# Optimization experiments

Hardware: AMD Instinct MI355X
Metric: run time of the kernel (lower is better)

Reference implementation:

```python
import jax, jax.numpy as jnp
import numpy as np

N = 200000
D = 128
PARAM_SCALE = 1.0 / D  # keep exp() exponent bounded (original torch.rand init overflows at scale)


def setup_inputs() -> dict:
    key = jax.random.key(0)
    kx, k1, k2, k3, k4 = jax.random.split(key, 5)
    X = jax.random.normal(kx, (N, D), dtype=jnp.float32)
    W_sum = jax.random.uniform(k1, (D, D), dtype=jnp.float32) * PARAM_SCALE
    W_alpha = jax.random.uniform(k2, (D, D), dtype=jnp.float32) * PARAM_SCALE
    a_alpha = jax.random.uniform(k3, (D, 1), dtype=jnp.float32) * PARAM_SCALE
    b_alpha = jax.random.uniform(k4, (D, 1), dtype=jnp.float32) * PARAM_SCALE
    return {"X": X, "W_sum": W_sum, "W_alpha": W_alpha,
            "a_alpha": a_alpha, "b_alpha": b_alpha}


def reference(X, W_sum, W_alpha, a_alpha, b_alpha):
    # a_w = a_alpha^T @ W_alpha, b_w = b_alpha^T @ W_alpha  -> (D,) each
    a_w = a_alpha[:, 0] @ W_alpha
    b_w = b_alpha[:, 0] @ W_alpha
    # alpha_j = exp(a_w . X[0] + b_w . X[j])  -> (N,)
    alpha = jnp.exp(a_w @ X[0] + X @ b_w)
    # weighted sum over all rows, normalized by sum of (unnormalized) weights
    sum_output = (alpha @ X) / jnp.sum(alpha)  # (D,)
    return sum_output @ W_sum  # (D,)
```

## Files before the change

### kernel.cpp

```cpp
#include <hip/hip_runtime.h>
#include <hip/hip_bf16.h>

#define D 128


__global__ __launch_bounds__(256) void prep_kernel(
    const float* __restrict__ W_alpha,
    const float* __restrict__ b_alpha,
    float* __restrict__ bw_out)
{
    const int t  = threadIdx.x;
    const int kk = blockIdx.x * 16 + (t & 15);
    const int gg = t >> 4;
    float s = 0.f;
    #pragma unroll
    for (int i = gg * 8; i < gg * 8 + 8; ++i)
        s = fmaf(b_alpha[i], W_alpha[i * D + kk], s);
    __shared__ float sA[16][17];
    sA[gg][t & 15] = s;
    __syncthreads();
    if (t < 16) {
        float r = 0.f;
        #pragma unroll
        for (int g2 = 0; g2 < 16; ++g2) r += sA[g2][t];
        bw_out[blockIdx.x * 16 + t] = r;
    }
}

__global__ __launch_bounds__(256, 8) void main_pass_kernel(
    const float* __restrict__ X,
    const float* __restrict__ bw,
    float* __restrict__ partial_wsum,
    float* __restrict__ partial_alpha,
    int nrows)
{
    const int t    = threadIdx.x;
    const int col4 = t & 31;
    const int rg   = t >> 5;

    const float4 bwv = reinterpret_cast<const float4*>(bw)[col4];

    float a0 = 0.f, a1 = 0.f, a2 = 0.f, a3 = 0.f;
    float aacc = 0.f;

    const int ftiles = nrows >> 4;
    const float4* __restrict__ X4 = reinterpret_cast<const float4*>(X);
    const int    gstep = gridDim.x;
    const size_t step  = (size_t)gstep * 512;

    int tile = blockIdx.x;
    if (tile < ftiles) {
        size_t addr = ((size_t)tile * 16 + rg * 2) * 32 + col4;
        float4 x0 = X4[addr];
        float4 x1 = X4[addr + 32];

        while (tile < ftiles) {
            const int ntile = tile + gstep;
            const size_t naddr = addr + (ntile < ftiles ? step : (size_t)0);
            const float4 n0 = X4[naddr];
            const float4 n1 = X4[naddr + 32];

            float d0 = fmaf(x0.x, bwv.x, fmaf(x0.y, bwv.y, fmaf(x0.z, bwv.z, x0.w * bwv.w)));
            float d1 = fmaf(x1.x, bwv.x, fmaf(x1.y, bwv.y, fmaf(x1.z, bwv.z, x1.w * bwv.w)));
            #pragma unroll
            for (int m = 16; m >= 1; m >>= 1) {
                d0 += __shfl_xor(d0, m, 64);
                d1 += __shfl_xor(d1, m, 64);
            }
            const float al0 = __expf(d0);
            const float al1 = __expf(d1);
            aacc += al0 + al1;
            a0 = fmaf(al0, x0.x, fmaf(al1, x1.x, a0));
            a1 = fmaf(al0, x0.y, fmaf(al1, x1.y, a1));
            a2 = fmaf(al0, x0.z, fmaf(al1, x1.z, a2));
            a3 = fmaf(al0, x0.w, fmaf(al1, x1.w, a3));

            x0 = n0; x1 = n1; addr = naddr; tile = ntile;
        }
    }

    const int rem = nrows & 15;
    if (rem && blockIdx.x == 0) {
        const int r0 = (nrows & ~15) + rg * 2;
        if (r0 < nrows) {
            const float4 x0r = X4[(size_t)r0 * 32 + col4];
            const bool v1 = (r0 + 1) < nrows;
            const float4 x1r = v1 ? X4[(size_t)(r0 + 1) * 32 + col4]
                                  : make_float4(0.f, 0.f, 0.f, 0.f);
            float d0 = fmaf(x0r.x, bwv.x, fmaf(x0r.y, bwv.y, fmaf(x0r.z, bwv.z, x0r.w * bwv.w)));
            float d1 = fmaf(x1r.x, bwv.x, fmaf(x1r.y, bwv.y, fmaf(x1r.z, bwv.z, x1r.w * bwv.w)));
            #pragma unroll
            for (int m = 16; m >= 1; m >>= 1) {
                d0 += __shfl_xor(d0, m, 64);
                d1 += __shfl_xor(d1, m, 64);
            }
            const float al0 = __expf(d0);
            const float al1 = v1 ? __expf(d1) : 0.f;
            aacc += al0 + al1;
            a0 = fmaf(al0, x0r.x, fmaf(al1, x1r.x, a0));
            a1 = fmaf(al0, x0r.y, fmaf(al1, x1r.y, a1));
            a2 = fmaf(al0, x0r.z, fmaf(al1, x1r.z, a2));
            a3 = fmaf(al0, x0r.w, fmaf(al1, x1r.w, a3));
        }
    }

    __shared__ float red[8][32][4];
    __shared__ float reda[8];
    red[rg][col4][0] = a0;
    red[rg][col4][1] = a1;
    red[rg][col4][2] = a2;
    red[rg][col4][3] = a3;
    if (col4 == 0) reda[rg] = aacc;
    __syncthreads();

    if (t < D) {
        float s = 0.f;
        #pragma unroll
        for (int r = 0; r < 8; ++r) s += red[r][t >> 2][t & 3];
        partial_wsum[(size_t)blockIdx.x * D + t] = s;
    }
    if (t == 0) {
        float s = 0.f;
        #pragma unroll
        for (int r = 0; r < 8; ++r) s += reda[r];
        partial_alpha[blockIdx.x] = s;
    }
}

__global__ __launch_bounds__(512) void r1m_kernel(
    const float* __restrict__ partial_wsum,
    const float* __restrict__ partial_alpha,
    const float* __restrict__ W_sum,
    float* __restrict__ ovec,
    float* __restrict__ ga,
    int NB)
{
    const int b  = blockIdx.x;
    const int t  = threadIdx.x;
    const int k  = t & 127;
    const int rs = t >> 7;
    const int nper = NB >> 6;

    double s = 0.0;
    for (int j = rs; j < nper; j += 4)
        s += (double)partial_wsum[(size_t)(b + 64 * j) * D + k];
    __shared__ double red[4][D];
    red[rs][k] = s;

    double ap = 0.0;
    if (t < 64) {
        for (int j = t; j < nper; j += 64)
            ap += (double)partial_alpha[b + 64 * j];
        #pragma unroll
        for (int m = 32; m >= 1; m >>= 1) ap += __shfl_xor(ap, m, 64);
        if (t == 0) ga[b] = (float)ap;
    }
    __syncthreads();

    __shared__ float mid_sh[D];
    if (t < D) mid_sh[t] = (float)(red[0][t] + red[1][t] + red[2][t] + red[3][t]);
    __syncthreads();

    float o = 0.f;
    #pragma unroll 8
    for (int kk = rs * 32; kk < rs * 32 + 32; ++kk)
        o = fmaf(mid_sh[kk], W_sum[kk * D + k], o);
    __shared__ float rout[4][D];
    rout[rs][k] = o;
    __syncthreads();
    if (t < D)
        ovec[(size_t)b * D + t] = rout[0][t] + rout[1][t] + rout[2][t] + rout[3][t];
}

__global__ __launch_bounds__(256) void fin_kernel(
    const float* __restrict__ ovec,
    const float* __restrict__ ga,
    float* __restrict__ out)
{
    const int t = threadIdx.x;
    const int k = t & 127;
    const int h = t >> 7;

    double s = 0.0;
    for (int b = h; b < 64; b += 2)
        s += (double)ovec[(size_t)b * D + k];
    __shared__ double red[2][D];
    red[h][k] = s;

    __shared__ double asum_sh;
    if (t < 64) {
        double a = (double)ga[t];
        #pragma unroll
        for (int m = 32; m >= 1; m >>= 1) a += __shfl_xor(a, m, 64);
        if (t == 0) asum_sh = a;
    }
    __syncthreads();

    if (t < D)
        out[t] = (float)((red[0][t] + red[1][t]) / asum_sh);
}

extern "C" void kernel_launch(void* const* d_in, const int* in_sizes, int n_in,
                              void* d_out, int out_size, void* d_ws, size_t ws_size,
                              hipStream_t stream) {
    const float* X       = (const float*)d_in[0];
    const float* W_sum   = (const float*)d_in[1];
    const float* W_alpha = (const float*)d_in[2];
    const float* b_alpha = (const float*)d_in[4];
    float* out = (float*)d_out;

    const int nrows = in_sizes[0] / D;

    int NB = 2048;
    auto need = [&](int nb) {
        return (size_t)nb * (D + 1) * sizeof(float)
             + 256
             + (size_t)64 * (D + 1) * sizeof(float)
             + (D + 4) * sizeof(float);
    };
    while (NB > 64 && need(NB) > ws_size) NB >>= 1;

    char* ws = (char*)d_ws;
    float* pw   = (float*)ws;
    float* pa   = pw + (size_t)NB * D;
    size_t off = ((size_t)NB * (D + 1) * sizeof(float) + 255) & ~(size_t)255;
    float* ovec = (float*)(ws + off);
    float* ga   = ovec + (size_t)64 * D;
    float* bw   = ga + 64;

    prep_kernel<<<8, 256, 0, stream>>>(W_alpha, b_alpha, bw);
    main_pass_kernel<<<NB, 256, 0, stream>>>(X, bw, pw, pa, nrows);
    r1m_kernel<<<64, 512, 0, stream>>>(pw, pa, W_sum, ovec, ga, NB);
    fin_kernel<<<1, 256, 0, stream>>>(ovec, ga, out);
}
```

Measured before the change: 40.22 us.

## Fuse final reduction into r1m via fixed-point atomics and last-block ticket

Removes the separate fin_kernel launch. Each r1m block now adds its projected partial output and alpha sum into 64-bit fixed-point atomic accumulators, and the last block to arrive (found with a global ticket counter) does the final division. prep_kernel becomes a single 1024-thread block that also zeroes the accumulators, and W_sum is staged into 64KB of LDS with float4 loads. The goal is to save one kernel launch and its gap, at the cost of atomics, fixed-point rounding error, and a large LDS footprint that lowers occupancy in r1m.

```diff
diff --git a/kernel.cpp b/kernel.cpp
--- a/kernel.cpp
+++ b/kernel.cpp
@@ -2,28 +2,39 @@
 #include <hip/hip_bf16.h>
 
 #define D 128
-
-
-__global__ __launch_bounds__(256) void prep_kernel(
+#define FIXS 1099511627776.0
+
+
+__global__ __launch_bounds__(1024) void prep_kernel(
     const float* __restrict__ W_alpha,
     const float* __restrict__ b_alpha,
-    float* __restrict__ bw_out)
+    float* __restrict__ bw_out,
+    long long* __restrict__ oacc,
+    int* __restrict__ gcnt)
 {
-    const int t  = threadIdx.x;
-    const int kk = blockIdx.x * 16 + (t & 15);
-    const int gg = t >> 4;
-    float s = 0.f;
+    const int t = threadIdx.x;
+    if (t < D + 1) oacc[t] = 0;
+    if (t == D + 1) gcnt[0] = 0;
+
+    const int k = t & 127;
+    const int g = t >> 7;
+    __shared__ float bal[D];
+    if (t < D) bal[t] = b_alpha[t];
+    __syncthreads();
+
+    float bw = 0.f;
     #pragma unroll
-    for (int i = gg * 8; i < gg * 8 + 8; ++i)
-        s = fmaf(b_alpha[i], W_alpha[i * D + kk], s);
-    __shared__ float sA[16][17];
-    sA[gg][t & 15] = s;
-    __syncthreads();
-    if (t < 16) {
-        float r = 0.f;
-        #pragma unroll
-        for (int g2 = 0; g2 < 16; ++g2) r += sA[g2][t];
-        bw_out[blockIdx.x * 16 + t] = r;
+    for (int i = g * 16; i < g * 16 + 16; ++i)
+        bw = fmaf(bal[i], W_alpha[i * D + k], bw);
+
+    __shared__ float rbw[8][D];
+    rbw[g][k] = bw;
+    __syncthreads();
+    if (t < D) {
+        float B = 0.f;
+        #pragma unroll
+        for (int r = 0; r < 8; ++r) B += rbw[r][t];
+        bw_out[t] = B;
     }
 }
 
@@ -127,12 +138,13 @@
     }
 }
 
-__global__ __launch_bounds__(512) void r1m_kernel(
+__global__ __launch_bounds__(512) void r1mf_kernel(
     const float* __restrict__ partial_wsum,
     const float* __restrict__ partial_alpha,
     const float* __restrict__ W_sum,
-    float* __restrict__ ovec,
-    float* __restrict__ ga,
+    long long* __restrict__ oacc,
+    int* __restrict__ gcnt,
+    float* __restrict__ out,
     int NB)
 {
     const int b  = blockIdx.x;
@@ -141,63 +153,79 @@
     const int rs = t >> 7;
     const int nper = NB >> 6;
 
+    const float4* __restrict__ W4 = reinterpret_cast<const float4*>(W_sum);
+    float4 w[8];
+    #pragma unroll
+    for (int i = 0; i < 8; ++i) w[i] = W4[t + 512 * i];
+
     double s = 0.0;
+    #pragma unroll 4
     for (int j = rs; j < nper; j += 4)
         s += (double)partial_wsum[(size_t)(b + 64 * j) * D + k];
     __shared__ double red[4][D];
     red[rs][k] = s;
 
-    double ap = 0.0;
+    __shared__ float ga_sh;
     if (t < 64) {
+        double ap = 0.0;
         for (int j = t; j < nper; j += 64)
             ap += (double)partial_alpha[b + 64 * j];
         #pragma unroll
         for (int m = 32; m >= 1; m >>= 1) ap += __shfl_xor(ap, m, 64);
-        if (t == 0) ga[b] = (float)ap;
-    }
+        if (t == 0) ga_sh = (float)ap;
+    }
+
+    __shared__ float wls[D * D];
+    float4* wls4 = reinterpret_cast<float4*>(wls);
+    #pragma unroll
+    for (int i = 0; i < 8; ++i) wls4[t + 512 * i] = w[i];
     __syncthreads();
 
     __shared__ float mid_sh[D];
-    if (t < D) mid_sh[t] = (float)(red[0][t] + red[1][t] + red[2][t] + red[3][t]);
+    if (t < D)
+        mid_sh[t] = (float)(red[0][t] + red[1][t] + red[2][t] + red[3][t]);
     __syncthreads();
 
     float o = 0.f;
     #pragma unroll 8
     for (int kk = rs * 32; kk < rs * 32 + 32; ++kk)
-        o = fmaf(mid_sh[kk], W_sum[kk * D + k], o);
+        o = fmaf(mid_sh[kk], wls[kk * D + k], o);
     __shared__ float rout[4][D];
     rout[rs][k] = o;
     __syncthreads();
-    if (t < D)
-        ovec[(size_t)b * D + t] = rout[0][t] + rout[1][t] + rout[2][t] + rout[3][t];
-}
-
-__global__ __launch_bounds__(256) void fin_kernel(
-    const float* __restrict__ ovec,
-    const float* __restrict__ ga,
-    float* __restrict__ out)
-{
-    const int t = threadIdx.x;
-    const int k = t & 127;
-    const int h = t >> 7;
-
-    double s = 0.0;
-    for (int b = h; b < 64; b += 2)
-        s += (double)ovec[(size_t)b * D + k];
-    __shared__ double red[2][D];
-    red[h][k] = s;
-
-    __shared__ double asum_sh;
-    if (t < 64) {
-        double a = (double)ga[t];
-        #pragma unroll
-        for (int m = 32; m >= 1; m >>= 1) a += __shfl_xor(a, m, 64);
-        if (t == 0) asum_sh = a;
-    }
-    __syncthreads();
-
-    if (t < D)
-        out[t] = (float)((red[0][t] + red[1][t]) / asum_sh);
+
+    if (t < D) {
+        const float of = rout[0][t] + rout[1][t] + rout[2][t] + rout[3][t];
+        const long long fx = (long long)llrint((double)of * FIXS);
+        __hip_atomic_fetch_add(&oacc[t], fx, __ATOMIC_RELAXED,
+                               __HIP_MEMORY_SCOPE_AGENT);
+    }
+    if (t == 0) {
+        const long long fa = (long long)llrint((double)ga_sh * FIXS);
+        __hip_atomic_fetch_add(&oacc[D], fa, __ATOMIC_RELAXED,
+                               __HIP_MEMORY_SCOPE_AGENT);
+    }
+    __syncthreads();
+
+    __shared__ int tick_sh;
+    if (t == 0) {
+        __threadfence();
+        tick_sh = __hip_atomic_fetch_add(gcnt, 1, __ATOMIC_ACQ_REL,
+                                         __HIP_MEMORY_SCOPE_AGENT);
+    }
+    __syncthreads();
+    if (tick_sh != 63) return;
+
+    __shared__ double asum_d;
+    if (t == 0)
+        asum_d = (double)__hip_atomic_load(&oacc[D], __ATOMIC_RELAXED,
+                                           __HIP_MEMORY_SCOPE_AGENT);
+    __syncthreads();
+    if (t < D) {
+        const long long num = __hip_atomic_load(&oacc[t], __ATOMIC_RELAXED,
+                                                __HIP_MEMORY_SCOPE_AGENT);
+        out[t] = (float)((double)num / asum_d);
+    }
 }
 
 extern "C" void kernel_launch(void* const* d_in, const int* in_sizes, int n_in,
@@ -214,22 +242,22 @@
     int NB = 2048;
     auto need = [&](int nb) {
         return (size_t)nb * (D + 1) * sizeof(float)
-             + 256
-             + (size_t)64 * (D + 1) * sizeof(float)
-             + (D + 4) * sizeof(float);
+             + 256 + (D + 4) * sizeof(float)
+             + 256 + (D + 1) * sizeof(long long)
+             + sizeof(int) + 64;
     };
     while (NB > 64 && need(NB) > ws_size) NB >>= 1;
 
     char* ws = (char*)d_ws;
-    float* pw   = (float*)ws;
-    float* pa   = pw + (size_t)NB * D;
+    float* pw = (float*)ws;
+    float* pa = pw + (size_t)NB * D;
     size_t off = ((size_t)NB * (D + 1) * sizeof(float) + 255) & ~(size_t)255;
-    float* ovec = (float*)(ws + off);
-    float* ga   = ovec + (size_t)64 * D;
-    float* bw   = ga + 64;
-
-    prep_kernel<<<8, 256, 0, stream>>>(W_alpha, b_alpha, bw);
+    float* bw = (float*)(ws + off);
+    size_t off2 = (off + (D + 4) * sizeof(float) + 255) & ~(size_t)255;
+    long long* oacc = (long long*)(ws + off2);
+    int* gcnt = (int*)(oacc + (D + 1));
+
+    prep_kernel<<<1, 1024, 0, stream>>>(W_alpha, b_alpha, bw, oacc, gcnt);
     main_pass_kernel<<<NB, 256, 0, stream>>>(X, bw, pw, pa, nrows);
-    r1m_kernel<<<64, 512, 0, stream>>>(pw, pa, W_sum, ovec, ga, NB);
-    fin_kernel<<<1, 256, 0, stream>>>(ovec, ga, out);
-}
+    r1mf_kernel<<<64, 512, 0, stream>>>(pw, pa, W_sum, oacc, gcnt, out, NB);
+}
```

Measured after the change: 32.97 us. 1.22x faster.
